# Kernel optimization log

Hardware: AMD Instinct MI355X
Metric: run time of the kernel (lower is better)

Reference implementation:

```python
import jax, jax.numpy as jnp
import numpy as np

N = 8192

def gcn_conv(x, edge_index, W, b):
    # PyG GCNConv: x' = D^{-1/2} (A + I) D^{-1/2} (x W) + b
    n = x.shape[0]
    loops = jnp.arange(n, dtype=edge_index.dtype)
    src = jnp.concatenate([edge_index[0], loops])
    dst = jnp.concatenate([edge_index[1], loops])
    h = x @ W  # transform first (as PyG does): [n, out]
    deg = jax.ops.segment_sum(jnp.ones_like(dst, dtype=h.dtype), dst, num_segments=n)
    dinv = jnp.where(deg > 0, jax.lax.rsqrt(deg), 0.0)
    norm = dinv[src] * dinv[dst]  # [E+n]
    out = jax.ops.segment_sum(norm[:, None] * h[src], dst, num_segments=n)
    return out + b


def setup_inputs() -> dict:
    key = jax.random.key(0)
    ks = jax.random.split(key, 9)
    F, H = 512, 512
    E = 262144
    x = jax.random.normal(ks[0], (N, F), dtype=jnp.float32)
    o = jax.random.normal(ks[1], (N, 4), dtype=jnp.float32)
    edge_index = jax.random.randint(ks[2], (2, E), 0, N, dtype=jnp.int64)
    s = 1.0 / np.sqrt(F)
    W1 = jax.random.uniform(ks[3], (F, H), jnp.float32, -s, s)
    b1 = jnp.zeros((H,), jnp.float32)
    s2 = 1.0 / np.sqrt(H)
    W2 = jax.random.uniform(ks[4], (H, 1), jnp.float32, -s2, s2)
    b2 = jnp.zeros((1,), jnp.float32)
    Wl = jax.random.uniform(ks[5], (4, 1), jnp.float32, -0.5, 0.5)
    bl = jnp.zeros((1,), jnp.float32)
    return {"x": x, "o": o, "edge_index": edge_index,
            "W1": W1, "b1": b1, "W2": W2, "b2": b2, "Wl": Wl, "bl": bl}


def reference(x, o, edge_index, W1, b1, W2, b2, Wl, bl):
    h = gcn_conv(x, edge_index, W1, b1)
    h = jax.nn.relu(h)
    h = gcn_conv(h, edge_index, W2, b2)  # [N, 1]
    h = h.mean(axis=1)                    # [N]
    ohe = o @ Wl + bl                      # [N, 1]
    # faithful to torch: [N] + [N,1] broadcasts to [N,N]
    return h + ohe
```

## Files before the change

kernel.cpp:

```cpp
#include <hip/hip_runtime.h>

#define NN 8192
#define FI 512
#define FH 512
#define RS 128

typedef __attribute__((ext_vector_type(8))) short short8;
typedef __attribute__((ext_vector_type(4))) float f32x4;
typedef __attribute__((ext_vector_type(2))) float f32x2;

__device__ __forceinline__ unsigned short f2bf(float f) {
    unsigned u = __float_as_uint(f);
    unsigned r = (u + 0x7fff + ((u >> 16) & 1)) >> 16;
    return (unsigned short)r;
}

#define GLOAD_LDS16(g, l)                                                        \
    __builtin_amdgcn_global_load_lds((__attribute__((address_space(1))) const void*)(g), \
                                     (__attribute__((address_space(3))) void*)(l), 16, 0, 0)

__global__ void k_zero(int* __restrict__ zero_base) {
    zero_base[blockIdx.x * 256 + threadIdx.x] = 0;
}

__global__ __launch_bounds__(256) void k_prepdeg(const float* __restrict__ x,
                                                 const float* __restrict__ W1,
                                                 const int* __restrict__ dstE, int E,
                                                 const float* __restrict__ o,
                                                 const float* __restrict__ Wl,
                                                 const float* __restrict__ bl,
                                                 unsigned short* __restrict__ xb,
                                                 unsigned short* __restrict__ W1t,
                                                 int* __restrict__ deg,
                                                 float* __restrict__ ohe) {
    int b = blockIdx.x, t = threadIdx.x;
    int degB = (E + 255) >> 8;
    if (b < 1024) {
        #pragma unroll
        for (int u = 0; u < 4; ++u) {
            int i = (b * 4 + u) * 256 + t;
            float4 v = reinterpret_cast<const float4*>(x)[i];
            ushort4 h;
            h.x = f2bf(v.x); h.y = f2bf(v.y); h.z = f2bf(v.z); h.w = f2bf(v.w);
            reinterpret_cast<ushort4*>(xb)[i] = h;
        }
    } else if (b < 1088) {
        __shared__ float tile[64][65];
        int bi = (b - 1024) >> 3;
        int bj = (b - 1024) & 7;
        int c = t & 63, r0 = t >> 6;
        #pragma unroll
        for (int rr = 0; rr < 16; ++rr) {
            int row = rr * 4 + r0;
            tile[row][c] = W1[(size_t)(bi * 64 + row) * FH + bj * 64 + c];
        }
        __syncthreads();
        #pragma unroll
        for (int rr = 0; rr < 16; ++rr) {
            int row = rr * 4 + r0;
            W1t[(size_t)(bj * 64 + row) * FI + bi * 64 + c] = f2bf(tile[c][row]);
        }
    } else if (b < 1088 + degB) {
        int i = (b - 1088) * 256 + t;
        if (i < E) atomicAdd(&deg[dstE[i]], 1);
    } else {
        int v = (b - 1088 - degB) * 256 + t;
        float4 ov = *reinterpret_cast<const float4*>(&o[(size_t)v * 4]);
        ohe[v] = ov.x * Wl[0] + ov.y * Wl[1] + ov.z * Wl[2] + ov.w * Wl[3] + bl[0];
    }
}

__global__ __launch_bounds__(256) void k_fillgemm(const int* __restrict__ srcE,
                                                  const int* __restrict__ dstE, int E,
                                                  const int* __restrict__ deg,
                                                  int* __restrict__ cursor,
                                                  int2* __restrict__ csr,
                                                  const unsigned short* __restrict__ xb,
                                                  const unsigned short* __restrict__ W1t,
                                                  unsigned char* __restrict__ h8) {
    __shared__ __align__(16) unsigned short As[64 * 64];
    __shared__ __align__(16) unsigned short Bs[64 * 64];
    int bid = blockIdx.x, tid = threadIdx.x;

    if (bid < 1056) {
        int i = bid * 256 + tid;
        if (i < E) {
            int s = srcE[i], d = dstE[i];
            float w = rsqrtf((float)(deg[s] + 1)) * rsqrtf((float)(deg[d] + 1));
            int slot = atomicAdd(&cursor[d], 1);
            if (slot < RS) csr[(d << 7) + slot] = make_int2(s, __float_as_int(w));
        } else if (i < E + NN) {
            int v = i - E;
            float dv = rsqrtf((float)(deg[v] + 1));
            int slot = atomicAdd(&cursor[v], 1);
            if (slot < RS) csr[(v << 7) + slot] = make_int2(v, __float_as_int(dv * dv));
        }
        return;
    }

    int q0 = bid - 1056;
    int lane = tid & 63;
    int wave = tid >> 6;
    int wm = wave >> 1, wn = wave & 1;
    int bm = (q0 >> 3) * 64, bn = (q0 & 7) * 64;

    f32x4 acc[2][2] = {};
    int r  = lane & 15;
    int s0 = lane >> 4;

    for (int kt = 0; kt < FI / 64; ++kt) {
        #pragma unroll
        for (int t = 0; t < 2; ++t) {
            int q   = t * 256 + tid;
            int row = q >> 3;
            int sl  = q & 7;
            int sg  = sl ^ (row & 7);
            GLOAD_LDS16(xb  + (size_t)(bm + row) * FI + kt * 64 + sg * 8, As + q * 8);
            GLOAD_LDS16(W1t + (size_t)(bn + row) * FI + kt * 64 + sg * 8, Bs + q * 8);
        }
        __syncthreads();

        #pragma unroll
        for (int kc = 0; kc < 2; ++kc) {
            short8 a[2], b[2];
            #pragma unroll
            for (int m = 0; m < 2; ++m) {
                int row = wm * 32 + m * 16 + r;
                int sl  = (kc * 4 + s0) ^ (row & 7);
                a[m] = *reinterpret_cast<const short8*>(As + row * 64 + sl * 8);
            }
            #pragma unroll
            for (int n = 0; n < 2; ++n) {
                int row = wn * 32 + n * 16 + r;
                int sl  = (kc * 4 + s0) ^ (row & 7);
                b[n] = *reinterpret_cast<const short8*>(Bs + row * 64 + sl * 8);
            }
            #pragma unroll
            for (int m = 0; m < 2; ++m)
                #pragma unroll
                for (int n = 0; n < 2; ++n)
                    acc[m][n] = __builtin_amdgcn_mfma_f32_16x16x32_bf16(a[m], b[n], acc[m][n], 0, 0, 0);
        }
        __syncthreads();
    }

    #pragma unroll
    for (int m = 0; m < 2; ++m) {
        #pragma unroll
        for (int n = 0; n < 2; ++n) {
            int col = bn + wn * 32 + n * 16 + (lane & 15);
            int rw0 = bm + wm * 32 + m * 16 + (lane >> 4) * 4;
            #pragma unroll
            for (int reg = 0; reg < 4; ++reg) {
                float v = acc[m][n][reg];
                int pk = __builtin_amdgcn_cvt_pk_fp8_f32(v, v, 0, false);
                h8[(size_t)(rw0 + reg) * FH + col] = (unsigned char)(pk & 0xff);
            }
        }
    }
}

__device__ __forceinline__ void accp(f32x2* __restrict__ acc, uint2 rv, float w) {
    f32x2 wv = {w, w};
    acc[0] += wv * __builtin_amdgcn_cvt_pk_f32_fp8((int)rv.x, false);
    acc[1] += wv * __builtin_amdgcn_cvt_pk_f32_fp8((int)rv.x, true);
    acc[2] += wv * __builtin_amdgcn_cvt_pk_f32_fp8((int)rv.y, false);
    acc[3] += wv * __builtin_amdgcn_cvt_pk_f32_fp8((int)rv.y, true);
}

__global__ __launch_bounds__(256) void k_agg(const unsigned char* __restrict__ h8,
                                             const int* __restrict__ deg,
                                             const int2* __restrict__ csr,
                                             const float* __restrict__ b1,
                                             const float* __restrict__ W2,
                                             float* __restrict__ z) {
    int lane = threadIdx.x & 63;
    int v = blockIdx.x * 4 + (threadIdx.x >> 6);
    f32x2 acc[4] = {};
    int p0 = v << 7;
    int cnt_all = deg[v] + 1; if (cnt_all > RS) cnt_all = RS;
    int p1 = p0 + cnt_all;
    for (int base = p0; base < p1; base += 64) {
        int cnt = p1 - base; if (cnt > 64) cnt = 64;
        int2 sw = (lane < cnt) ? csr[base + lane] : make_int2(0, 0);
        int j = 0;
        for (; j + 4 <= cnt; j += 4) {
            int   s0 = __shfl(sw.x, j),     s1 = __shfl(sw.x, j + 1);
            int   s2 = __shfl(sw.x, j + 2), s3 = __shfl(sw.x, j + 3);
            float w0 = __int_as_float(__shfl(sw.y, j));
            float w1 = __int_as_float(__shfl(sw.y, j + 1));
            float w2 = __int_as_float(__shfl(sw.y, j + 2));
            float w3 = __int_as_float(__shfl(sw.y, j + 3));
            uint2 r0 = *reinterpret_cast<const uint2*>(h8 + (size_t)s0 * FH + lane * 8);
            uint2 r1 = *reinterpret_cast<const uint2*>(h8 + (size_t)s1 * FH + lane * 8);
            uint2 r2 = *reinterpret_cast<const uint2*>(h8 + (size_t)s2 * FH + lane * 8);
            uint2 r3 = *reinterpret_cast<const uint2*>(h8 + (size_t)s3 * FH + lane * 8);
            accp(acc, r0, w0);
            accp(acc, r1, w1);
            accp(acc, r2, w2);
            accp(acc, r3, w3);
        }
        for (; j < cnt; ++j) {
            int   sj = __shfl(sw.x, j);
            float wj = __int_as_float(__shfl(sw.y, j));
            uint2 rj = *reinterpret_cast<const uint2*>(h8 + (size_t)sj * FH + lane * 8);
            accp(acc, rj, wj);
        }
    }
    const f32x2* b2p = reinterpret_cast<const f32x2*>(b1 + lane * 8);
    const f32x2* w2p = reinterpret_cast<const f32x2*>(W2 + lane * 8);
    float val = 0.f;
    #pragma unroll
    for (int q = 0; q < 4; ++q) {
        f32x2 t = acc[q] + b2p[q];
        t.x = fmaxf(t.x, 0.f);
        t.y = fmaxf(t.y, 0.f);
        f32x2 r = t * w2p[q];
        val += r.x + r.y;
    }
    #pragma unroll
    for (int off = 32; off; off >>= 1) val += __shfl_down(val, off);
    if (lane == 0) z[v] = val;
}

__global__ __launch_bounds__(256) void k_nodeout(const float* __restrict__ z,
                                                 const int* __restrict__ deg,
                                                 const int2* __restrict__ csr,
                                                 const float* __restrict__ b2,
                                                 const float* __restrict__ ohe,
                                                 float4* __restrict__ out) {
    __shared__ float h2s[64];
    int s = blockIdx.x & 127;
    int r = blockIdx.x >> 7;
    int t = threadIdx.x;

    {
        int node = s * 64 + (t >> 2);
        int q = t & 3;
        int p0 = node << 7;
        int cnt = deg[node] + 1; if (cnt > RS) cnt = RS;
        float acc = 0.f;
        for (int p = p0 + q; p < p0 + cnt; p += 4) {
            int2 sw = csr[p];
            acc += __int_as_float(sw.y) * z[sw.x];
        }
        acc += __shfl_down(acc, 1);
        acc += __shfl_down(acc, 2);
        if (q == 0) h2s[t >> 2] = acc + b2[0];
    }
    __syncthreads();

    int rowLocal = t >> 4;
    int colq     = t & 15;
    float4 hv = reinterpret_cast<const float4*>(h2s)[colq];
    int i0 = r * 256;
    #pragma unroll
    for (int pass = 0; pass < 16; ++pass) {
        int i = i0 + pass * 16 + rowLocal;
        float oi = ohe[i];
        out[(size_t)i * 2048 + s * 16 + colq] =
            make_float4(hv.x + oi, hv.y + oi, hv.z + oi, hv.w + oi);
    }
}

extern "C" void kernel_launch(void* const* d_in, const int* in_sizes, int n_in,
                              void* d_out, int out_size, void* d_ws, size_t ws_size,
                              hipStream_t stream) {
    const float* x  = (const float*)d_in[0];
    const float* o  = (const float*)d_in[1];
    const int*   ei = (const int*)d_in[2];
    const float* W1 = (const float*)d_in[3];
    const float* b1 = (const float*)d_in[4];
    const float* W2 = (const float*)d_in[5];
    const float* b2 = (const float*)d_in[6];
    const float* Wl = (const float*)d_in[7];
    const float* bl = (const float*)d_in[8];
    float* out = (float*)d_out;

    const int E = in_sizes[2] / 2;
    const int* src = ei;
    const int* dst = ei + E;
    const int degB = (E + 255) >> 8;

    char* p = (char*)d_ws;
    auto alloc = [&](size_t bytes) {
        char* r = p;
        p += (bytes + 255) & ~(size_t)255;
        return r;
    };
    int*   deg     = (int*)  alloc(NN * 4);
    int*   cursor  = (int*)  alloc(NN * 4);
    int2*  csr     = (int2*) alloc((size_t)NN * RS * 8);
    unsigned short* xb  = (unsigned short*)alloc((size_t)NN * FI * 2);
    unsigned short* W1t = (unsigned short*)alloc((size_t)FH * FI * 2);
    unsigned char*  h8  = (unsigned char*) alloc((size_t)NN * FH);
    float* z       = (float*)alloc(NN * 4);
    float* ohe     = (float*)alloc(NN * 4);

    k_zero    <<<64, 256, 0, stream>>>(deg);
    k_prepdeg <<<1088 + degB + 32, 256, 0, stream>>>(x, W1, dst, E, o, Wl, bl,
                                                     xb, W1t, deg, ohe);
    k_fillgemm<<<1056 + 1024, 256, 0, stream>>>(src, dst, E, deg, cursor, csr,
                                                xb, W1t, h8);
    k_agg     <<<NN / 4, 256, 0, stream>>>(h8, deg, csr, b1, W2, z);
    k_nodeout <<<4096, 256, 0, stream>>>(z, deg, csr, b2, ohe, (float4*)out);
}
```

Measured before the change: 119.5 us.

## Drop separate degree pass; derive degrees from CSR fill cursor and compute norms on the fly

Removes the zeroing kernel and the atomic degree-counting pass. The fill cursor's final count (in-degree plus self loop) now serves as the degree, and cursor zeroing moves into the prep kernel. The CSR stores only source indices instead of (src, weight) pairs, which halves its footprint. Edge normalisation weights are recomputed in the aggregation kernels from cursor reads and rsqrt, trading one launch and the atomic pass for extra gathered cursor loads per edge.

```diff
diff --git a/kernel.cpp b/kernel.cpp
--- a/kernel.cpp
+++ b/kernel.cpp
@@ -19,22 +19,16 @@
     __builtin_amdgcn_global_load_lds((__attribute__((address_space(1))) const void*)(g), \
                                      (__attribute__((address_space(3))) void*)(l), 16, 0, 0)
 
-__global__ void k_zero(int* __restrict__ zero_base) {
-    zero_base[blockIdx.x * 256 + threadIdx.x] = 0;
-}
-
-__global__ __launch_bounds__(256) void k_prepdeg(const float* __restrict__ x,
-                                                 const float* __restrict__ W1,
-                                                 const int* __restrict__ dstE, int E,
-                                                 const float* __restrict__ o,
-                                                 const float* __restrict__ Wl,
-                                                 const float* __restrict__ bl,
-                                                 unsigned short* __restrict__ xb,
-                                                 unsigned short* __restrict__ W1t,
-                                                 int* __restrict__ deg,
-                                                 float* __restrict__ ohe) {
+__global__ __launch_bounds__(256) void k_prep(const float* __restrict__ x,
+                                              const float* __restrict__ W1,
+                                              const float* __restrict__ o,
+                                              const float* __restrict__ Wl,
+                                              const float* __restrict__ bl,
+                                              unsigned short* __restrict__ xb,
+                                              unsigned short* __restrict__ W1t,
+                                              float* __restrict__ ohe,
+                                              int* __restrict__ cursor) {
     int b = blockIdx.x, t = threadIdx.x;
-    int degB = (E + 255) >> 8;
     if (b < 1024) {
         #pragma unroll
         for (int u = 0; u < 4; ++u) {
@@ -60,21 +54,19 @@
             int row = rr * 4 + r0;
             W1t[(size_t)(bj * 64 + row) * FI + bi * 64 + c] = f2bf(tile[c][row]);
         }
-    } else if (b < 1088 + degB) {
-        int i = (b - 1088) * 256 + t;
-        if (i < E) atomicAdd(&deg[dstE[i]], 1);
-    } else {
-        int v = (b - 1088 - degB) * 256 + t;
+    } else if (b < 1120) {
+        int v = (b - 1088) * 256 + t;
         float4 ov = *reinterpret_cast<const float4*>(&o[(size_t)v * 4]);
         ohe[v] = ov.x * Wl[0] + ov.y * Wl[1] + ov.z * Wl[2] + ov.w * Wl[3] + bl[0];
+    } else {
+        cursor[(b - 1120) * 256 + t] = 0;
     }
 }
 
 __global__ __launch_bounds__(256) void k_fillgemm(const int* __restrict__ srcE,
                                                   const int* __restrict__ dstE, int E,
-                                                  const int* __restrict__ deg,
                                                   int* __restrict__ cursor,
-                                                  int2* __restrict__ csr,
+                                                  int* __restrict__ csr_src,
                                                   const unsigned short* __restrict__ xb,
                                                   const unsigned short* __restrict__ W1t,
                                                   unsigned char* __restrict__ h8) {
@@ -86,14 +78,12 @@
         int i = bid * 256 + tid;
         if (i < E) {
             int s = srcE[i], d = dstE[i];
-            float w = rsqrtf((float)(deg[s] + 1)) * rsqrtf((float)(deg[d] + 1));
             int slot = atomicAdd(&cursor[d], 1);
-            if (slot < RS) csr[(d << 7) + slot] = make_int2(s, __float_as_int(w));
+            if (slot < RS) csr_src[(d << 7) + slot] = s;
         } else if (i < E + NN) {
             int v = i - E;
-            float dv = rsqrtf((float)(deg[v] + 1));
             int slot = atomicAdd(&cursor[v], 1);
-            if (slot < RS) csr[(v << 7) + slot] = make_int2(v, __float_as_int(dv * dv));
+            if (slot < RS) csr_src[(v << 7) + slot] = v;
         }
         return;
     }
@@ -169,8 +159,8 @@
 }
 
 __global__ __launch_bounds__(256) void k_agg(const unsigned char* __restrict__ h8,
-                                             const int* __restrict__ deg,
-                                             const int2* __restrict__ csr,
+                                             const int* __restrict__ cursor,
+                                             const int* __restrict__ csr_src,
                                              const float* __restrict__ b1,
                                              const float* __restrict__ W2,
                                              float* __restrict__ z) {
@@ -178,19 +168,22 @@
     int v = blockIdx.x * 4 + (threadIdx.x >> 6);
     f32x2 acc[4] = {};
     int p0 = v << 7;
-    int cnt_all = deg[v] + 1; if (cnt_all > RS) cnt_all = RS;
+    int cnt_true = cursor[v];
+    float dinv_d = rsqrtf((float)cnt_true);
+    int cnt_all = cnt_true > RS ? RS : cnt_true;
     int p1 = p0 + cnt_all;
     for (int base = p0; base < p1; base += 64) {
         int cnt = p1 - base; if (cnt > 64) cnt = 64;
-        int2 sw = (lane < cnt) ? csr[base + lane] : make_int2(0, 0);
+        int   sl = (lane < cnt) ? csr_src[base + lane] : 0;
+        float ws = rsqrtf((float)cursor[sl]);
         int j = 0;
         for (; j + 4 <= cnt; j += 4) {
-            int   s0 = __shfl(sw.x, j),     s1 = __shfl(sw.x, j + 1);
-            int   s2 = __shfl(sw.x, j + 2), s3 = __shfl(sw.x, j + 3);
-            float w0 = __int_as_float(__shfl(sw.y, j));
-            float w1 = __int_as_float(__shfl(sw.y, j + 1));
-            float w2 = __int_as_float(__shfl(sw.y, j + 2));
-            float w3 = __int_as_float(__shfl(sw.y, j + 3));
+            int   s0 = __shfl(sl, j),     s1 = __shfl(sl, j + 1);
+            int   s2 = __shfl(sl, j + 2), s3 = __shfl(sl, j + 3);
+            float w0 = __shfl(ws, j)     * dinv_d;
+            float w1 = __shfl(ws, j + 1) * dinv_d;
+            float w2 = __shfl(ws, j + 2) * dinv_d;
+            float w3 = __shfl(ws, j + 3) * dinv_d;
             uint2 r0 = *reinterpret_cast<const uint2*>(h8 + (size_t)s0 * FH + lane * 8);
             uint2 r1 = *reinterpret_cast<const uint2*>(h8 + (size_t)s1 * FH + lane * 8);
             uint2 r2 = *reinterpret_cast<const uint2*>(h8 + (size_t)s2 * FH + lane * 8);
@@ -201,8 +194,8 @@
             accp(acc, r3, w3);
         }
         for (; j < cnt; ++j) {
-            int   sj = __shfl(sw.x, j);
-            float wj = __int_as_float(__shfl(sw.y, j));
+            int   sj = __shfl(sl, j);
+            float wj = __shfl(ws, j) * dinv_d;
             uint2 rj = *reinterpret_cast<const uint2*>(h8 + (size_t)sj * FH + lane * 8);
             accp(acc, rj, wj);
         }
@@ -224,8 +217,8 @@
 }
 
 __global__ __launch_bounds__(256) void k_nodeout(const float* __restrict__ z,
-                                                 const int* __restrict__ deg,
-                                                 const int2* __restrict__ csr,
+                                                 const int* __restrict__ cursor,
+                                                 const int* __restrict__ csr_src,
                                                  const float* __restrict__ b2,
                                                  const float* __restrict__ ohe,
                                                  float4* __restrict__ out) {
@@ -238,11 +231,14 @@
         int node = s * 64 + (t >> 2);
         int q = t & 3;
         int p0 = node << 7;
-        int cnt = deg[node] + 1; if (cnt > RS) cnt = RS;
+        int cnt_true = cursor[node];
+        float dinv_d = rsqrtf((float)cnt_true);
+        int cnt = cnt_true > RS ? RS : cnt_true;
         float acc = 0.f;
         for (int p = p0 + q; p < p0 + cnt; p += 4) {
-            int2 sw = csr[p];
-            acc += __int_as_float(sw.y) * z[sw.x];
+            int sv = csr_src[p];
+            float w = rsqrtf((float)cursor[sv]) * dinv_d;
+            acc += w * z[sv];
         }
         acc += __shfl_down(acc, 1);
         acc += __shfl_down(acc, 2);
@@ -280,7 +276,6 @@
     const int E = in_sizes[2] / 2;
     const int* src = ei;
     const int* dst = ei + E;
-    const int degB = (E + 255) >> 8;
 
     char* p = (char*)d_ws;
     auto alloc = [&](size_t bytes) {
@@ -288,20 +283,17 @@
         p += (bytes + 255) & ~(size_t)255;
         return r;
     };
-    int*   deg     = (int*)  alloc(NN * 4);
-    int*   cursor  = (int*)  alloc(NN * 4);
-    int2*  csr     = (int2*) alloc((size_t)NN * RS * 8);
+    int*  cursor  = (int*) alloc(NN * 4);
+    int*  csr_src = (int*) alloc((size_t)NN * RS * 4);
     unsigned short* xb  = (unsigned short*)alloc((size_t)NN * FI * 2);
     unsigned short* W1t = (unsigned short*)alloc((size_t)FH * FI * 2);
     unsigned char*  h8  = (unsigned char*) alloc((size_t)NN * FH);
     float* z       = (float*)alloc(NN * 4);
     float* ohe     = (float*)alloc(NN * 4);
 
-    k_zero    <<<64, 256, 0, stream>>>(deg);
-    k_prepdeg <<<1088 + degB + 32, 256, 0, stream>>>(x, W1, dst, E, o, Wl, bl,
-                                                     xb, W1t, deg, ohe);
-    k_fillgemm<<<1056 + 1024, 256, 0, stream>>>(src, dst, E, deg, cursor, csr,
+    k_prep    <<<1152, 256, 0, stream>>>(x, W1, o, Wl, bl, xb, W1t, ohe, cursor);
+    k_fillgemm<<<1056 + 1024, 256, 0, stream>>>(src, dst, E, cursor, csr_src,
                                                 xb, W1t, h8);
-    k_agg     <<<NN / 4, 256, 0, stream>>>(h8, deg, csr, b1, W2, z);
-    k_nodeout <<<4096, 256, 0, stream>>>(z, deg, csr, b2, ohe, (float4*)out);
-}
+    k_agg     <<<NN / 4, 256, 0, stream>>>(h8, cursor, csr_src, b1, W2, z);
+    k_nodeout <<<4096, 256, 0, stream>>>(z, cursor, csr_src, b2, ohe, (float4*)out);
+}
```

Result: no change. 119.3 us (-0.2%).
